# Performance work log

Measured on AMD Instinct MI355X. Metric: run time of the kernel, lower is better.

The kernel has to match this reference:

```python
import jax, jax.numpy as jnp
import numpy as np

NEG = 10000.0

def setup_inputs() -> dict:
    key = jax.random.key(0)
    ks = jax.random.split(key, 5)
    B, S, D = 2, 2048, 1024
    std = 1.0 / np.sqrt(D)
    return {
        "x": jax.random.normal(ks[0], (B, S, D), dtype=jnp.float32),
        "Wq": jax.random.normal(ks[1], (D, D), dtype=jnp.float32) * std,
        "bq": jnp.zeros((D,), jnp.float32),
        "Wk": jax.random.normal(ks[2], (D, D), dtype=jnp.float32) * std,
        "bk": jnp.zeros((D,), jnp.float32),
        "Wv": jax.random.normal(ks[3], (D, D), dtype=jnp.float32) * std,
        "bv": jnp.zeros((D,), jnp.float32),
        "Wo": jax.random.normal(ks[4], (D, D), dtype=jnp.float32) * std,
        "bo": jnp.zeros((D,), jnp.float32),
    }

def reference(x, Wq, bq, Wk, bk, Wv, bv, Wo, bo):
    # Linear projections + relu activation (as in the keras layer; note: no head split
    # is performed in this implementation, head_num is only a divisibility check).
    q = jax.nn.relu(x @ Wq + bq)  # [B,S,D]
    k = jax.nn.relu(x @ Wk + bk)
    v = jax.nn.relu(x @ Wv + bv)
    D = q.shape[-1]
    e = jnp.einsum('bqd,bkd->bqk', q, k) / jnp.sqrt(jnp.float32(D))  # [B,S,S]
    # history_only causal mask: penalize key positions j > query position i
    S = e.shape[-1]
    causal = (jnp.arange(S)[None, :] > jnp.arange(S)[:, None]).astype(e.dtype)
    e = e - NEG * causal[None, :, :]
    # stable softmax exactly as in the source (max-subtract, exp, normalize)
    e = jnp.exp(e - jnp.max(e, axis=-1, keepdims=True))
    attn = e / jnp.sum(e, axis=-1, keepdims=True)
    y = jnp.einsum('bqk,bkd->bqd', attn, v)
    return jax.nn.relu(y @ Wo + bo)
```

## Files before the change

### kernel.cpp

```cpp
#include <hip/hip_runtime.h>
#include <math.h>


typedef _Float16 f16x8 __attribute__((ext_vector_type(8)));
typedef float f32x4 __attribute__((ext_vector_type(4)));

#define BK 64

__device__ __forceinline__ void gload_lds16(const void* g, void* l) {
  __builtin_amdgcn_global_load_lds(
      (const __attribute__((address_space(1))) void*)g,
      (__attribute__((address_space(3))) void*)l, 16, 0, 0);
}

template<int TMp, int TNp>
__device__ __forceinline__ void gemm_acc(
    const _Float16* __restrict__ A, const _Float16* __restrict__ BT,
    _Float16* Ah, _Float16* Bh, int sAr, int sBr, int kend, int m0, int n0,
    f32x4 (&acc)[TMp / 32][TNp / 32])
{
  const int tid  = threadIdx.x;
  const int lane = tid & 63;
  const int wid  = tid >> 6;
  const int wm   = (wid >> 1) * (TMp / 2);
  const int wn   = (wid & 1) * (TNp / 2);
  const int l15  = lane & 15;
  const int quad = lane >> 4;
  constexpr int MT = TMp / 32;
  constexpr int NT = TNp / 32;
  constexpr int AI = TMp / 32;
  constexpr int BI = TNp / 32;
  const int r8  = lane >> 3;
  const int swc = ((lane & 7) ^ r8) * 8;
  const int arow = wid * (TMp / 4);
  const int brow = wid * (TNp / 4);

  for (int k0 = 0; k0 < kend; k0 += BK) {
    #pragma unroll
    for (int t = 0; t < AI; ++t)
      gload_lds16(A + (long long)(m0 + arow + t * 8 + r8) * sAr + k0 + swc,
                  Ah + (arow + t * 8) * BK);
    #pragma unroll
    for (int t = 0; t < BI; ++t)
      gload_lds16(BT + (long long)(n0 + brow + t * 8 + r8) * sBr + k0 + swc,
                  Bh + (brow + t * 8) * BK);
    __syncthreads();

    const int c0 = (quad ^ (l15 & 7)) * 8;
    const _Float16* ar = Ah + (wm + l15) * BK;
    const _Float16* br = Bh + (wn + l15) * BK;
    f16x8 af[MT][2], bf[NT][2];
    #pragma unroll
    for (int t = 0; t < MT; ++t) {
      af[t][0] = *(const f16x8*)(ar + t * 16 * BK + c0);
      af[t][1] = *(const f16x8*)(ar + t * 16 * BK + (c0 ^ 32));
    }
    #pragma unroll
    for (int t = 0; t < NT; ++t) {
      bf[t][0] = *(const f16x8*)(br + t * 16 * BK + c0);
      bf[t][1] = *(const f16x8*)(br + t * 16 * BK + (c0 ^ 32));
    }
    #pragma unroll
    for (int ks = 0; ks < 2; ++ks)
      #pragma unroll
      for (int mt = 0; mt < MT; ++mt)
        #pragma unroll
        for (int nt = 0; nt < NT; ++nt)
          acc[mt][nt] = __builtin_amdgcn_mfma_f32_16x16x32_f16(
              af[mt][ks], bf[nt][ks], acc[mt][nt], 0, 0, 0);
    __syncthreads();
  }
}

template<int TMp, int TNp, bool RELU, bool HAS_BIAS, typename OT>
__device__ __forceinline__ void gemm_store(
    f32x4 (&acc)[TMp / 32][TNp / 32], const float* __restrict__ bias,
    OT* __restrict__ C, int Nout, float scale, int m0, int n0)
{
  const int tid  = threadIdx.x;
  const int lane = tid & 63;
  const int wid  = tid >> 6;
  const int wm   = (wid >> 1) * (TMp / 2);
  const int wn   = (wid & 1) * (TNp / 2);
  const int l15  = lane & 15;
  const int quad = lane >> 4;
  constexpr int MT = TMp / 32;
  constexpr int NT = TNp / 32;

  float bvals[NT];
  if (HAS_BIAS) {
    #pragma unroll
    for (int nt = 0; nt < NT; ++nt)
      bvals[nt] = bias[n0 + wn + nt * 16 + l15];
  }
  #pragma unroll
  for (int mt = 0; mt < MT; ++mt) {
    #pragma unroll
    for (int nt = 0; nt < NT; ++nt) {
      const int col = n0 + wn + nt * 16 + l15;
      #pragma unroll
      for (int r = 0; r < 4; ++r) {
        const int row = m0 + wm + mt * 16 + quad * 4 + r;
        float v = acc[mt][nt][r] * scale;
        if (HAS_BIAS) v += bvals[nt];
        if (RELU) v = fmaxf(v, 0.f);
        C[(long long)row * Nout + col] = (OT)v;
      }
    }
  }
}

__global__ __launch_bounds__(256) void qkv_kernel(
    const _Float16* __restrict__ xh, const _Float16* __restrict__ Wcat,
    const float* __restrict__ bq, const float* __restrict__ bk,
    const float* __restrict__ bv,
    _Float16* __restrict__ Qh, _Float16* __restrict__ Kh,
    _Float16* __restrict__ Vh, int D)
{
  __shared__ _Float16 Ah[128 * BK];
  __shared__ _Float16 Bh[128 * BK];
  const int m0  = blockIdx.y * 128;
  const int n0g = blockIdx.x * 128;
  f32x4 acc[4][4];
  #pragma unroll
  for (int i = 0; i < 4; ++i)
    #pragma unroll
    for (int j = 0; j < 4; ++j) acc[i][j] = (f32x4){0.f, 0.f, 0.f, 0.f};

  gemm_acc<128, 128>(xh, Wcat, Ah, Bh, D, D, D, m0, n0g, acc);

  const int mat = n0g >> 10;
  const int c0  = n0g & 1023;
  _Float16* C = (mat == 0) ? Qh : (mat == 1) ? Kh : Vh;
  const float* bias = (mat == 0) ? bq : (mat == 1) ? bk : bv;
  gemm_store<128, 128, true, true, _Float16>(acc, bias, C, D, 1.0f, m0, c0);
}

__global__ __launch_bounds__(256) void mid_kernel(
    const _Float16* __restrict__ Qh, const _Float16* __restrict__ Kh,
    _Float16* __restrict__ E, const _Float16* __restrict__ WoT,
    const _Float16* __restrict__ Vh, _Float16* __restrict__ VWT,
    int S, int D)
{
  __shared__ _Float16 Ah[128 * BK];
  __shared__ _Float16 Bh[128 * BK];
  for (int id = blockIdx.x; id < 528; id += 512) {
    const _Float16 *A, *BT;
    _Float16* C;
    int m0, n0;
    float scale;
    if (id < 272) {
      const int z = (id >= 136);
      const int t = id - z * 136;
      int i = (int)((sqrtf(8.f * t + 1.f) - 1.f) * 0.5f);
      while ((i + 1) * (i + 2) / 2 <= t) ++i;
      while (i * (i + 1) / 2 > t) --i;
      const int j = t - i * (i + 1) / 2;
      m0 = i * 128;
      n0 = j * 128;
      A  = Qh + (long long)z * S * D;
      BT = Kh + (long long)z * S * D;
      C  = E + (long long)z * S * S;
      scale = 0.03125f;
    } else {
      const int t = id - 272;
      const int z = t >> 7;
      const int u = t & 127;
      m0 = (u >> 4) * 128;
      n0 = (u & 15) * 128;
      A  = WoT;
      BT = Vh + (long long)z * S * D;
      C  = VWT + (long long)z * D * S;
      scale = 1.0f;
    }
    f32x4 acc[4][4];
    #pragma unroll
    for (int i = 0; i < 4; ++i)
      #pragma unroll
      for (int j = 0; j < 4; ++j) acc[i][j] = (f32x4){0.f, 0.f, 0.f, 0.f};

    gemm_acc<128, 128>(A, BT, Ah, Bh, D, D, D, m0, n0, acc);
    gemm_store<128, 128, false, false, _Float16>(acc, nullptr, C, S, scale,
                                                 m0, n0);
  }
}

__global__ __launch_bounds__(256) void pv_kernel(
    const _Float16* __restrict__ E, const _Float16* __restrict__ VWT,
    const float* __restrict__ bo, float* __restrict__ out, int S, int D)
{
  __shared__ _Float16 Ah[64 * BK];
  __shared__ _Float16 Bh[128 * BK];
  const int z  = blockIdx.z;
  const int m0 = ((int)gridDim.y - 1 - (int)blockIdx.y) * 64;
  const int n0 = blockIdx.x * 128;
  const _Float16* A  = E + (long long)z * S * S;
  const _Float16* BT = VWT + (long long)z * D * S;
  float* C = out + (long long)z * S * D;
  const int kend = m0 + 64;

  f32x4 acc[2][4];
  #pragma unroll
  for (int i = 0; i < 2; ++i)
    #pragma unroll
    for (int j = 0; j < 4; ++j) acc[i][j] = (f32x4){0.f, 0.f, 0.f, 0.f};

  gemm_acc<64, 128>(A, BT, Ah, Bh, S, S, kend, m0, n0, acc);
  gemm_store<64, 128, true, true, float>(acc, bo, C, D, 1.0f, m0, n0);
}

__global__ __launch_bounds__(256) void prep_kernel(
    const float* __restrict__ x, _Float16* __restrict__ xh,
    const float* __restrict__ W0, const float* __restrict__ W1,
    const float* __restrict__ W2, const float* __restrict__ W3,
    _Float16* __restrict__ Wcat, int D)
{
  const int id = blockIdx.x;
  const int tid = threadIdx.x;
  if (id < 2048) {
    const long long i = ((long long)id * 256 + tid) * 8;
    float4 a = *(const float4*)(x + i);
    float4 b = *(const float4*)(x + i + 4);
    f16x8 o = {(_Float16)a.x, (_Float16)a.y, (_Float16)a.z, (_Float16)a.w,
               (_Float16)b.x, (_Float16)b.y, (_Float16)b.z, (_Float16)b.w};
    *(f16x8*)(xh + i) = o;
    return;
  }
  __shared__ _Float16 t[64][72];
  const int u = id - 2048;
  const int z = u >> 8;
  const int v = u & 255;
  const float* W = (z == 0) ? W0 : (z == 1) ? W1 : (z == 2) ? W2 : W3;
  _Float16* dst = Wcat + (long long)z * D * D;
  const int k0 = (v >> 4) * 64, n0 = (v & 15) * 64;
  #pragma unroll
  for (int it = 0; it < 4; ++it) {
    int idx = tid + it * 256;
    int r = idx >> 4, c4 = (idx & 15) << 2;
    float4 w = *(const float4*)(W + (long long)(k0 + r) * D + n0 + c4);
    t[r][c4 + 0] = (_Float16)w.x; t[r][c4 + 1] = (_Float16)w.y;
    t[r][c4 + 2] = (_Float16)w.z; t[r][c4 + 3] = (_Float16)w.w;
  }
  __syncthreads();
  #pragma unroll
  for (int it = 0; it < 2; ++it) {
    int idx = tid + it * 256;
    int r = idx >> 3, c8 = (idx & 7) << 3;
    f16x8 o;
    #pragma unroll
    for (int j = 0; j < 8; ++j) o[j] = t[c8 + j][r];
    *(f16x8*)(dst + (long long)(n0 + r) * D + k0 + c8) = o;
  }
}

__global__ __launch_bounds__(256) void softmax_causal_h(
    _Float16* __restrict__ E, int S)
{
  const int i = blockIdx.x;
  _Float16* row = E + ((long long)blockIdx.y * S + i) * S;
  const int tid = threadIdx.x;
  const int n = i + 1;
  const int j0 = tid * 8;

  f16x8 hv = *(const f16x8*)(row + j0);
  float vals[8];
  float m = -3.0e38f;
  #pragma unroll
  for (int t = 0; t < 8; ++t) {
    float v = (j0 + t < n) ? (float)hv[t] : -3.0e38f;
    vals[t] = v;
    m = fmaxf(m, v);
  }
  #pragma unroll
  for (int o = 32; o > 0; o >>= 1) m = fmaxf(m, __shfl_down(m, o, 64));

  __shared__ float rmax[4];
  __shared__ float rsum[4];
  const int wave = tid >> 6;
  if ((tid & 63) == 0) rmax[wave] = m;
  __syncthreads();
  m = fmaxf(fmaxf(rmax[0], rmax[1]), fmaxf(rmax[2], rmax[3]));

  float s = 0.f;
  #pragma unroll
  for (int t = 0; t < 8; ++t) {
    float e = (j0 + t < n) ? expf(vals[t] - m) : 0.f;
    vals[t] = e;
    s += e;
  }
  #pragma unroll
  for (int o = 32; o > 0; o >>= 1) s += __shfl_down(s, o, 64);
  if ((tid & 63) == 0) rsum[wave] = s;
  __syncthreads();
  s = rsum[0] + rsum[1] + rsum[2] + rsum[3];

  const float inv = 1.0f / s;
  f16x8 ov;
  #pragma unroll
  for (int t = 0; t < 8; ++t) ov[t] = (_Float16)(vals[t] * inv);
  *(f16x8*)(row + j0) = ov;
}

extern "C" void kernel_launch(void* const* d_in, const int* in_sizes, int n_in,
                              void* d_out, int out_size, void* d_ws, size_t ws_size,
                              hipStream_t stream) {
  const float* x  = (const float*)d_in[0];
  const float* Wq = (const float*)d_in[1];
  const float* bq = (const float*)d_in[2];
  const float* Wk = (const float*)d_in[3];
  const float* bk = (const float*)d_in[4];
  const float* Wv = (const float*)d_in[5];
  const float* bv = (const float*)d_in[6];
  const float* Wo = (const float*)d_in[7];
  const float* bo = (const float*)d_in[8];
  float* out = (float*)d_out;

  const int Bn = 2, S = 2048, D = 1024;
  const int M = Bn * S;
  const size_t MD = (size_t)M * D;
  const size_t DD = (size_t)D * D;
  const size_t SS = (size_t)Bn * S * S;

  _Float16* ws   = (_Float16*)d_ws;
  _Float16* xh   = ws;
  _Float16* Wcat = xh + MD;
  _Float16* Qh   = Wcat + 4 * DD;
  _Float16* Kh   = Qh + MD;
  _Float16* Vh   = Kh + MD;
  _Float16* VWT  = Vh + MD;
  _Float16* E    = VWT + MD;

  dim3 blk(256);

  prep_kernel<<<dim3(3072), blk, 0, stream>>>(x, xh, Wq, Wk, Wv, Wo, Wcat, D);

  qkv_kernel<<<dim3(3 * D / 128, M / 128), blk, 0, stream>>>(
      xh, Wcat, bq, bk, bv, Qh, Kh, Vh, D);

  mid_kernel<<<dim3(512), blk, 0, stream>>>(
      Qh, Kh, E, Wcat + 3 * DD, Vh, VWT, S, D);

  softmax_causal_h<<<dim3(S, Bn), blk, 0, stream>>>(E, S);

  pv_kernel<<<dim3(D / 128, S / 64, Bn), blk, 0, stream>>>(
      E, VWT, bo, out, S, D);
}
```

Measured before the change: 203.6 us.

## Double-buffer LDS tiles in GEMM loop and launch one block per mid tile

The shared GEMM inner loop now keeps two LDS buffers and issues the global-to-LDS loads for the next K tile before computing on the current one, so load latency overlaps MFMA work and one barrier per iteration is dropped. LDS use doubles in the qkv, mid and pv kernels (up to 64KB per block), which may lower occupancy. mid_kernel also drops its grid-stride loop and launches 528 blocks, one per tile, instead of 512.

After: 201.6 us. About the same (-1.0%).

```diff
diff --git a/kernel.cpp b/kernel.cpp
--- a/kernel.cpp
+++ b/kernel.cpp
@@ -35,20 +35,28 @@
   const int arow = wid * (TMp / 4);
   const int brow = wid * (TNp / 4);
 
-  for (int k0 = 0; k0 < kend; k0 += BK) {
+  auto stage = [&](int k0, int buf) {
+    _Float16* Ad = Ah + buf * (TMp * BK);
+    _Float16* Bd = Bh + buf * (TNp * BK);
     #pragma unroll
     for (int t = 0; t < AI; ++t)
       gload_lds16(A + (long long)(m0 + arow + t * 8 + r8) * sAr + k0 + swc,
-                  Ah + (arow + t * 8) * BK);
+                  Ad + (arow + t * 8) * BK);
     #pragma unroll
     for (int t = 0; t < BI; ++t)
       gload_lds16(BT + (long long)(n0 + brow + t * 8 + r8) * sBr + k0 + swc,
-                  Bh + (brow + t * 8) * BK);
-    __syncthreads();
+                  Bd + (brow + t * 8) * BK);
+  };
+
+  stage(0, 0);
+  __syncthreads();
+  int cur = 0;
+  for (int k0 = 0; k0 < kend; k0 += BK) {
+    if (k0 + BK < kend) stage(k0 + BK, cur ^ 1);
 
     const int c0 = (quad ^ (l15 & 7)) * 8;
-    const _Float16* ar = Ah + (wm + l15) * BK;
-    const _Float16* br = Bh + (wn + l15) * BK;
+    const _Float16* ar = Ah + cur * (TMp * BK) + (wm + l15) * BK;
+    const _Float16* br = Bh + cur * (TNp * BK) + (wn + l15) * BK;
     f16x8 af[MT][2], bf[NT][2];
     #pragma unroll
     for (int t = 0; t < MT; ++t) {
@@ -68,7 +76,9 @@
         for (int nt = 0; nt < NT; ++nt)
           acc[mt][nt] = __builtin_amdgcn_mfma_f32_16x16x32_f16(
               af[mt][ks], bf[nt][ks], acc[mt][nt], 0, 0, 0);
+
     __syncthreads();
+    cur ^= 1;
   }
 }
 
@@ -117,8 +127,8 @@
     _Float16* __restrict__ Qh, _Float16* __restrict__ Kh,
     _Float16* __restrict__ Vh, int D)
 {
-  __shared__ _Float16 Ah[128 * BK];
-  __shared__ _Float16 Bh[128 * BK];
+  __shared__ _Float16 Ah[2 * 128 * BK];
+  __shared__ _Float16 Bh[2 * 128 * BK];
   const int m0  = blockIdx.y * 128;
   const int n0g = blockIdx.x * 128;
   f32x4 acc[4][4];
@@ -142,55 +152,54 @@
     const _Float16* __restrict__ Vh, _Float16* __restrict__ VWT,
     int S, int D)
 {
-  __shared__ _Float16 Ah[128 * BK];
-  __shared__ _Float16 Bh[128 * BK];
-  for (int id = blockIdx.x; id < 528; id += 512) {
-    const _Float16 *A, *BT;
-    _Float16* C;
-    int m0, n0;
-    float scale;
-    if (id < 272) {
-      const int z = (id >= 136);
-      const int t = id - z * 136;
-      int i = (int)((sqrtf(8.f * t + 1.f) - 1.f) * 0.5f);
-      while ((i + 1) * (i + 2) / 2 <= t) ++i;
-      while (i * (i + 1) / 2 > t) --i;
-      const int j = t - i * (i + 1) / 2;
-      m0 = i * 128;
-      n0 = j * 128;
-      A  = Qh + (long long)z * S * D;
-      BT = Kh + (long long)z * S * D;
-      C  = E + (long long)z * S * S;
-      scale = 0.03125f;
-    } else {
-      const int t = id - 272;
-      const int z = t >> 7;
-      const int u = t & 127;
-      m0 = (u >> 4) * 128;
-      n0 = (u & 15) * 128;
-      A  = WoT;
-      BT = Vh + (long long)z * S * D;
-      C  = VWT + (long long)z * D * S;
-      scale = 1.0f;
-    }
-    f32x4 acc[4][4];
-    #pragma unroll
-    for (int i = 0; i < 4; ++i)
-      #pragma unroll
-      for (int j = 0; j < 4; ++j) acc[i][j] = (f32x4){0.f, 0.f, 0.f, 0.f};
-
-    gemm_acc<128, 128>(A, BT, Ah, Bh, D, D, D, m0, n0, acc);
-    gemm_store<128, 128, false, false, _Float16>(acc, nullptr, C, S, scale,
-                                                 m0, n0);
-  }
+  __shared__ _Float16 Ah[2 * 128 * BK];
+  __shared__ _Float16 Bh[2 * 128 * BK];
+  const _Float16 *A, *BT;
+  _Float16* C;
+  int m0, n0;
+  float scale;
+  const int id = blockIdx.x;
+  if (id < 272) {
+    const int z = (id >= 136);
+    const int t = id - z * 136;
+    int i = (int)((sqrtf(8.f * t + 1.f) - 1.f) * 0.5f);
+    while ((i + 1) * (i + 2) / 2 <= t) ++i;
+    while (i * (i + 1) / 2 > t) --i;
+    const int j = t - i * (i + 1) / 2;
+    m0 = i * 128;
+    n0 = j * 128;
+    A  = Qh + (long long)z * S * D;
+    BT = Kh + (long long)z * S * D;
+    C  = E + (long long)z * S * S;
+    scale = 0.03125f;
+  } else {
+    const int t = id - 272;
+    const int z = t >> 7;
+    const int u = t & 127;
+    m0 = (u >> 4) * 128;
+    n0 = (u & 15) * 128;
+    A  = WoT;
+    BT = Vh + (long long)z * S * D;
+    C  = VWT + (long long)z * D * S;
+    scale = 1.0f;
+  }
+  f32x4 acc[4][4];
+  #pragma unroll
+  for (int i = 0; i < 4; ++i)
+    #pragma unroll
+    for (int j = 0; j < 4; ++j) acc[i][j] = (f32x4){0.f, 0.f, 0.f, 0.f};
+
+  gemm_acc<128, 128>(A, BT, Ah, Bh, D, D, D, m0, n0, acc);
+  gemm_store<128, 128, false, false, _Float16>(acc, nullptr, C, S, scale,
+                                               m0, n0);
 }
 
 __global__ __launch_bounds__(256) void pv_kernel(
     const _Float16* __restrict__ E, const _Float16* __restrict__ VWT,
     const float* __restrict__ bo, float* __restrict__ out, int S, int D)
 {
-  __shared__ _Float16 Ah[64 * BK];
-  __shared__ _Float16 Bh[128 * BK];
+  __shared__ _Float16 Ah[2 * 64 * BK];
+  __shared__ _Float16 Bh[2 * 128 * BK];
   const int z  = blockIdx.z;
   const int m0 = ((int)gridDim.y - 1 - (int)blockIdx.y) * 64;
   const int n0 = blockIdx.x * 128;
@@ -337,7 +346,7 @@
   qkv_kernel<<<dim3(3 * D / 128, M / 128), blk, 0, stream>>>(
       xh, Wcat, bq, bk, bv, Qh, Kh, Vh, D);
 
-  mid_kernel<<<dim3(512), blk, 0, stream>>>(
+  mid_kernel<<<dim3(528), blk, 0, stream>>>(
       Qh, Kh, E, Wcat + 3 * DD, Vh, VWT, S, D);
 
   softmax_causal_h<<<dim3(S, Bn), blk, 0, stream>>>(E, S);
```
